# Kernel tuning notes

Hardware: AMD Instinct MI355X
Metric: run time of the kernel (lower is better)

## Reference

```python
import jax, jax.numpy as jnp
import numpy as np
import math

N_NODES = 100000
N_EDGES = 3200000
F_IN = 512
HID = 128
N_CLS = 16


def setup_inputs() -> dict:
    key = jax.random.key(0)
    k = jax.random.split(key, 6)
    x = jax.random.normal(k[0], (N_NODES, F_IN), dtype=jnp.float32)
    edge_index = jax.random.randint(k[1], (2, N_EDGES), 0, N_NODES, dtype=jnp.int32)
    W1 = jax.random.normal(k[2], (F_IN, HID), dtype=jnp.float32) / np.sqrt(F_IN)
    W2 = jax.random.normal(k[3], (HID, HID), dtype=jnp.float32) / np.sqrt(HID)
    W3 = jax.random.normal(k[4], (N_CLS, HID), dtype=jnp.float32) / np.sqrt(HID)
    b3 = jnp.zeros((N_CLS,), dtype=jnp.float32)
    return {"x": x, "edge_index": edge_index, "W1": W1, "W2": W2, "W3": W3, "b3": b3}


def _sym_norm(edge_index, num_nodes, dtype):
    # add self loops with fill_value = trunc(log2(average_node_degree))
    E = edge_index.shape[1]
    fill = float(math.trunc(math.log2(E / num_nodes)))
    loops = jnp.arange(num_nodes, dtype=edge_index.dtype)
    row = jnp.concatenate([edge_index[0], loops])
    col = jnp.concatenate([edge_index[1], loops])
    w = jnp.concatenate([jnp.ones((E,), dtype), jnp.full((num_nodes,), fill, dtype)])
    deg = jax.ops.segment_sum(w, row, num_segments=num_nodes)
    deg_inv_sqrt = jnp.where(deg > 0, jax.lax.rsqrt(deg), 0.0)
    norm = deg_inv_sqrt[row] * w * deg_inv_sqrt[col]
    return row, col, norm


def reference(x, edge_index, W1, W2, W3, b3):
    N = x.shape[0]
    row, col, norm = _sym_norm(edge_index, N, x.dtype)

    def gcn(h, W):
        h = h @ W                                   # [N, d_out]
        msg = norm[:, None] * h[col]                # gather + scale, [E', d_out]
        return jax.ops.segment_sum(msg, row, num_segments=N)

    h = jax.nn.relu(gcn(x, W1))      # layer 1 + srelu (threshold clamped at 0)
    h = gcn(h, W2)                   # layer 2
    # dropout p=0.5 is identity in eval mode
    return h @ W3.T + b3             # linear classifier [N, n_classes]
```

## Files before the change

### kernel.cpp

```cpp
#include <hip/hip_runtime.h>
#include <cmath>

typedef __attribute__((ext_vector_type(8))) short short8;
typedef __attribute__((ext_vector_type(8))) unsigned short ushort8;
typedef __attribute__((ext_vector_type(4))) float f32x4;
typedef __attribute__((ext_vector_type(2))) float f32x2;
typedef __attribute__((ext_vector_type(4))) unsigned int uint4v;
typedef __attribute__((ext_vector_type(2))) int int2v;

#define EPB 4096
#define BCAP 20480

__device__ inline float bf16_lo(unsigned int p) {
  union { unsigned int i; float f; } v; v.i = p << 16; return v.f;
}
__device__ inline float bf16_hi(unsigned int p) {
  union { unsigned int i; float f; } v; v.i = p & 0xffff0000u; return v.f;
}
__device__ inline f32x2 bf2(unsigned int p) {
  union { unsigned int i; float f; } lo, hi;
  lo.i = p << 16;
  hi.i = p & 0xffff0000u;
  return (f32x2){lo.f, hi.f};
}
__device__ inline float bf16u(unsigned short w) {
  union { unsigned int i; float f; } v; v.i = (unsigned int)w << 16; return v.f;
}
__device__ inline unsigned short f32_to_bf16(float f) {
  union { float f; unsigned int i; } v; v.f = f;
  unsigned int x = v.i;
  x += 0x7fffu + ((x >> 16) & 1u);
  return (unsigned short)(x >> 16);
}
__device__ inline f32x2 pk_add(f32x2 a, f32x2 b) {
  f32x2 d;
  asm("v_pk_add_f32 %0, %1, %2" : "=v"(d) : "v"(a), "v"(b));
  return d;
}

__global__ __launch_bounds__(256) void bin_k(const int* __restrict__ rows,
                                             const int* __restrict__ cols,
                                             int* __restrict__ bucket_cursor,
                                             unsigned int* __restrict__ binned, int E) {
  __shared__ int lhist[256];
  __shared__ int gbase[256];
  __shared__ int loff[256];
  const int t = threadIdx.x;
  const int base = blockIdx.x * EPB;
  lhist[t] = 0;
  __syncthreads();

  int bk[16];
  unsigned int pk[16];
#pragma unroll
  for (int j = 0; j < 16; ++j) {
    int e = base + j * 256 + t;
    if (e < E) {
      int r = rows[e];
      int c = cols[e];
      bk[j] = r >> 9;
      pk[j] = ((unsigned int)(r & 511) << 17) | (unsigned int)c;
      atomicAdd(&lhist[bk[j]], 1);
    } else {
      bk[j] = -1;
    }
  }
  __syncthreads();
  if (lhist[t] > 0) gbase[t] = atomicAdd(&bucket_cursor[t], lhist[t]);
  loff[t] = 0;
  __syncthreads();
#pragma unroll
  for (int j = 0; j < 16; ++j) {
    if (bk[j] >= 0) {
      int rank = gbase[bk[j]] + atomicAdd(&loff[bk[j]], 1);
      if (rank < BCAP) binned[(size_t)bk[j] * BCAP + rank] = pk[j];
    }
  }
}

__global__ __launch_bounds__(1024) void bucket_csr_k(const unsigned int* __restrict__ binned,
                                                     const int* __restrict__ bucket_cursor,
                                                     int2v* __restrict__ rowse,
                                                     float* __restrict__ dis,
                                                     int* __restrict__ col_sorted,
                                                     int* __restrict__ perm,
                                                     int N, float fill) {
  __shared__ int lcnt[512];
  __shared__ int lscan[512];
  __shared__ int dh[512];
  __shared__ int ds2[512];
  const int b = blockIdx.x;
  const int t = threadIdx.x;
  const int start = b * BCAP;
  int cnt = bucket_cursor[b];
  if (cnt > BCAP) cnt = BCAP;
  const int endb = start + cnt;
  const int rbase = b << 9;

  if (t < 512) lcnt[t] = 0;
  __syncthreads();
  for (int i = start + t; i < endb; i += 1024)
    atomicAdd(&lcnt[binned[i] >> 17], 1);
  __syncthreads();

  int v = (t < 512) ? lcnt[t] : 0;
  if (t < 512) lscan[t] = v;
  __syncthreads();
  for (int off = 1; off < 512; off <<= 1) {
    int add = (t < 512 && t >= off) ? lscan[t - off] : 0;
    __syncthreads();
    if (t < 512) lscan[t] += add;
    __syncthreads();
  }

  if (t < 512) {
    int excl = lscan[t] - v;
    int r = rbase + t;
    if (r < N) {
      rowse[r] = (int2v){start + excl, start + excl + v};
      float d = (float)v + fill;
      dis[r] = d > 0.f ? rsqrtf(d) : 0.f;
    }
    lcnt[t] = excl;
  }

  if (t < 512) dh[t] = 0;
  __syncthreads();
  int key = 0;
  if (t < 512) {
    key = 511 - (v < 511 ? v : 511);
    atomicAdd(&dh[key], 1);
  }
  __syncthreads();
  if (t < 512) ds2[t] = dh[t];
  __syncthreads();
  for (int off = 1; off < 512; off <<= 1) {
    int add = (t < 512 && t >= off) ? ds2[t - off] : 0;
    __syncthreads();
    if (t < 512) ds2[t] += add;
    __syncthreads();
  }
  int base2 = 0;
  if (t < 512) base2 = ds2[t] - dh[t];
  __syncthreads();
  if (t < 512) dh[t] = base2;
  __syncthreads();
  if (t < 512) {
    int rank = atomicAdd(&dh[key], 1);
    perm[(b << 9) + rank] = rbase + t;
  }
  __syncthreads();

  for (int i = start + t; i < endb; i += 1024) {
    unsigned int pk = binned[i];
    int rl = (int)(pk >> 17);
    int c = (int)(pk & 0x1FFFFu);
    int pos = atomicAdd(&lcnt[rl], 1);
    col_sorted[start + pos] = c;
  }
}

__global__ __launch_bounds__(256) void cast_w_k(const float* __restrict__ W1,
                                                const float* __restrict__ W2,
                                                const float* __restrict__ W3,
                                                unsigned short* __restrict__ W1t,
                                                unsigned short* __restrict__ W2t,
                                                unsigned short* __restrict__ W3b,
                                                int FIN) {
  int g = blockIdx.x * 256 + threadIdx.x;
  int n1 = FIN * 128;
  if (g < n1) {
    int n = g & 127, k = g >> 7;
    W1t[n * FIN + k] = f32_to_bf16(W1[(size_t)k * 128 + n]);
  } else if (g < n1 + 128 * 128) {
    int gg = g - n1;
    int n = gg & 127, k = gg >> 7;
    W2t[n * 128 + k] = f32_to_bf16(W2[k * 128 + n]);
  } else if (g < n1 + 128 * 128 + 16 * 128) {
    int gg = g - n1 - 128 * 128;
    W3b[gg] = f32_to_bf16(W3[gg]);
  }
}

__global__ __launch_bounds__(256) void gemm_k(const void* __restrict__ Aq, int a_is_f32,
                                              int M, int K,
                                              const unsigned short* __restrict__ Bt,
                                              const float* __restrict__ dis,
                                              unsigned short* __restrict__ C) {
  __shared__ unsigned short Al[128 * 40];
  __shared__ unsigned short Bl[128 * 40];
  const int t = threadIdx.x;
  const int bm = blockIdx.x * 128;
  const int lane = t & 63;
  const int wave = t >> 6;
  const int wm = (wave >> 1) * 64;
  const int wn = (wave & 1) * 64;
  const int l15 = lane & 15;
  const int l4 = lane >> 4;

  f32x4 acc[4][4];
#pragma unroll
  for (int a = 0; a < 4; ++a)
#pragma unroll
    for (int b = 0; b < 4; ++b) acc[a][b] = (f32x4){0.f, 0.f, 0.f, 0.f};

  const int am = t >> 1;
  const int ak = (t & 1) * 16;
  const int bn = t >> 1;
  const int bk = (t & 1) * 16;
  const int arow = bm + am;
  const bool arow_ok = arow < M;

  auto load_a = [&](int k0, ushort8& o0, ushort8& o1) {
    o0 = (ushort8){0, 0, 0, 0, 0, 0, 0, 0};
    o1 = (ushort8){0, 0, 0, 0, 0, 0, 0, 0};
    if (arow_ok) {
      if (a_is_f32) {
        const float* p = (const float*)Aq + (size_t)arow * K + k0 + ak;
#pragma unroll
        for (int j = 0; j < 8; ++j) o0[j] = f32_to_bf16(p[j]);
#pragma unroll
        for (int j = 0; j < 8; ++j) o1[j] = f32_to_bf16(p[8 + j]);
      } else {
        const unsigned short* p = (const unsigned short*)Aq + (size_t)arow * K + k0 + ak;
        o0 = *(const ushort8*)p;
        o1 = *(const ushort8*)(p + 8);
      }
    }
  };

  ushort8 av0, av1;
  load_a(0, av0, av1);
  ushort8 bv0 = *(const ushort8*)(Bt + (size_t)bn * K + bk);
  ushort8 bv1 = *(const ushort8*)(Bt + (size_t)bn * K + bk + 8);

  for (int k0 = 0; k0 < K; k0 += 32) {
    *(ushort8*)&Al[am * 40 + ak] = av0;
    *(ushort8*)&Al[am * 40 + ak + 8] = av1;
    *(ushort8*)&Bl[bn * 40 + bk] = bv0;
    *(ushort8*)&Bl[bn * 40 + bk + 8] = bv1;
    __syncthreads();

    const int kn = k0 + 32;
    if (kn < K) {
      load_a(kn, av0, av1);
      bv0 = *(const ushort8*)(Bt + (size_t)bn * K + kn + bk);
      bv1 = *(const ushort8*)(Bt + (size_t)bn * K + kn + bk + 8);
    }

    short8 af[4];
#pragma unroll
    for (int mt = 0; mt < 4; ++mt)
      af[mt] = *(const short8*)&Al[(wm + mt * 16 + l15) * 40 + l4 * 8];
#pragma unroll
    for (int nt = 0; nt < 4; ++nt) {
      short8 bfr = *(const short8*)&Bl[(wn + nt * 16 + l15) * 40 + l4 * 8];
#pragma unroll
      for (int mt = 0; mt < 4; ++mt)
        acc[mt][nt] = __builtin_amdgcn_mfma_f32_16x16x32_bf16(af[mt], bfr, acc[mt][nt], 0, 0, 0);
    }
    __syncthreads();
  }

#pragma unroll
  for (int mt = 0; mt < 4; ++mt) {
    int rbase = bm + wm + mt * 16 + l4 * 4;
#pragma unroll
    for (int r = 0; r < 4; ++r) {
      int row = rbase + r;
      if (row < M) {
        float dr = dis[row];
#pragma unroll
        for (int nt = 0; nt < 4; ++nt) {
          int col = wn + nt * 16 + l15;
          C[(size_t)row * 128 + col] = f32_to_bf16(acc[mt][nt][r] * dr);
        }
      }
    }
  }
}

__global__ __launch_bounds__(256) void agg_k(const unsigned short* __restrict__ hs,
                                             const int2v* __restrict__ rowse,
                                             const int* __restrict__ cols,
                                             const float* __restrict__ dis,
                                             const int* __restrict__ perm,
                                             unsigned short* __restrict__ out_bf,
                                             const unsigned short* __restrict__ W3b,
                                             const float* __restrict__ b3,
                                             float* __restrict__ fcout,
                                             int N, float fill, int mode) {
  const int q = blockIdx.x * 16 + (threadIdx.x >> 4);
  const unsigned int fl = threadIdx.x & 15;
  const int rid = perm[q];
  if (rid >= N) return;
  const char* __restrict__ hsc = (const char*)hs;
  const unsigned int flo = fl << 4;

  int2v se = rowse[rid];
  int e = se.x;
  const int end = se.y;

  f32x2 a0 = {0.f, 0.f}, a1 = {0.f, 0.f}, a2 = {0.f, 0.f}, a3 = {0.f, 0.f};

  for (; e + 8 <= end; e += 8) {
    unsigned int c0 = (unsigned int)cols[e];
    unsigned int c1 = (unsigned int)cols[e + 1];
    unsigned int c2 = (unsigned int)cols[e + 2];
    unsigned int c3 = (unsigned int)cols[e + 3];
    unsigned int c4 = (unsigned int)cols[e + 4];
    unsigned int c5 = (unsigned int)cols[e + 5];
    unsigned int c6 = (unsigned int)cols[e + 6];
    unsigned int c7 = (unsigned int)cols[e + 7];
    uint4v p0 = *(const uint4v*)(hsc + ((c0 << 8) | flo));
    uint4v p1 = *(const uint4v*)(hsc + ((c1 << 8) | flo));
    uint4v p2 = *(const uint4v*)(hsc + ((c2 << 8) | flo));
    uint4v p3 = *(const uint4v*)(hsc + ((c3 << 8) | flo));
    uint4v p4 = *(const uint4v*)(hsc + ((c4 << 8) | flo));
    uint4v p5 = *(const uint4v*)(hsc + ((c5 << 8) | flo));
    uint4v p6 = *(const uint4v*)(hsc + ((c6 << 8) | flo));
    uint4v p7 = *(const uint4v*)(hsc + ((c7 << 8) | flo));
    a0 = pk_add(a0, bf2(p0[0])); a1 = pk_add(a1, bf2(p0[1]));
    a2 = pk_add(a2, bf2(p0[2])); a3 = pk_add(a3, bf2(p0[3]));
    a0 = pk_add(a0, bf2(p1[0])); a1 = pk_add(a1, bf2(p1[1]));
    a2 = pk_add(a2, bf2(p1[2])); a3 = pk_add(a3, bf2(p1[3]));
    a0 = pk_add(a0, bf2(p2[0])); a1 = pk_add(a1, bf2(p2[1]));
    a2 = pk_add(a2, bf2(p2[2])); a3 = pk_add(a3, bf2(p2[3]));
    a0 = pk_add(a0, bf2(p3[0])); a1 = pk_add(a1, bf2(p3[1]));
    a2 = pk_add(a2, bf2(p3[2])); a3 = pk_add(a3, bf2(p3[3]));
    a0 = pk_add(a0, bf2(p4[0])); a1 = pk_add(a1, bf2(p4[1]));
    a2 = pk_add(a2, bf2(p4[2])); a3 = pk_add(a3, bf2(p4[3]));
    a0 = pk_add(a0, bf2(p5[0])); a1 = pk_add(a1, bf2(p5[1]));
    a2 = pk_add(a2, bf2(p5[2])); a3 = pk_add(a3, bf2(p5[3]));
    a0 = pk_add(a0, bf2(p6[0])); a1 = pk_add(a1, bf2(p6[1]));
    a2 = pk_add(a2, bf2(p6[2])); a3 = pk_add(a3, bf2(p6[3]));
    a0 = pk_add(a0, bf2(p7[0])); a1 = pk_add(a1, bf2(p7[1]));
    a2 = pk_add(a2, bf2(p7[2])); a3 = pk_add(a3, bf2(p7[3]));
  }
  for (; e + 4 <= end; e += 4) {
    unsigned int c0 = (unsigned int)cols[e];
    unsigned int c1 = (unsigned int)cols[e + 1];
    unsigned int c2 = (unsigned int)cols[e + 2];
    unsigned int c3 = (unsigned int)cols[e + 3];
    uint4v p0 = *(const uint4v*)(hsc + ((c0 << 8) | flo));
    uint4v p1 = *(const uint4v*)(hsc + ((c1 << 8) | flo));
    uint4v p2 = *(const uint4v*)(hsc + ((c2 << 8) | flo));
    uint4v p3 = *(const uint4v*)(hsc + ((c3 << 8) | flo));
    a0 = pk_add(a0, bf2(p0[0])); a1 = pk_add(a1, bf2(p0[1]));
    a2 = pk_add(a2, bf2(p0[2])); a3 = pk_add(a3, bf2(p0[3]));
    a0 = pk_add(a0, bf2(p1[0])); a1 = pk_add(a1, bf2(p1[1]));
    a2 = pk_add(a2, bf2(p1[2])); a3 = pk_add(a3, bf2(p1[3]));
    a0 = pk_add(a0, bf2(p2[0])); a1 = pk_add(a1, bf2(p2[1]));
    a2 = pk_add(a2, bf2(p2[2])); a3 = pk_add(a3, bf2(p2[3]));
    a0 = pk_add(a0, bf2(p3[0])); a1 = pk_add(a1, bf2(p3[1]));
    a2 = pk_add(a2, bf2(p3[2])); a3 = pk_add(a3, bf2(p3[3]));
  }
  for (; e < end; ++e) {
    unsigned int c = (unsigned int)cols[e];
    uint4v p = *(const uint4v*)(hsc + ((c << 8) | flo));
    a0 = pk_add(a0, bf2(p[0])); a1 = pk_add(a1, bf2(p[1]));
    a2 = pk_add(a2, bf2(p[2])); a3 = pk_add(a3, bf2(p[3]));
  }

  uint4v ps = *(const uint4v*)(hsc + (((unsigned int)rid << 8) | flo));
  float dr = dis[rid];
  float v[8];
  v[0] = dr * (a0.x + fill * bf16_lo(ps[0]));
  v[1] = dr * (a0.y + fill * bf16_hi(ps[0]));
  v[2] = dr * (a1.x + fill * bf16_lo(ps[1]));
  v[3] = dr * (a1.y + fill * bf16_hi(ps[1]));
  v[4] = dr * (a2.x + fill * bf16_lo(ps[2]));
  v[5] = dr * (a2.y + fill * bf16_hi(ps[2]));
  v[6] = dr * (a3.x + fill * bf16_lo(ps[3]));
  v[7] = dr * (a3.y + fill * bf16_hi(ps[3]));

  if (mode == 0) {
    uint4v o;
#pragma unroll
    for (int k = 0; k < 4; ++k) {
      float f0 = fmaxf(v[2 * k], 0.f);
      float f1 = fmaxf(v[2 * k + 1], 0.f);
      o[k] = ((unsigned int)f32_to_bf16(f1) << 16) | (unsigned int)f32_to_bf16(f0);
    }
    *(uint4v*)((char*)out_bf + (((unsigned int)rid << 8) | flo)) = o;
  } else {
    float p[16];
#pragma unroll
    for (int c = 0; c < 16; ++c) {
      ushort8 wr = *(const ushort8*)(W3b + c * 128 + fl * 8);
      float s = v[0] * bf16u(wr[0]);
      s = fmaf(v[1], bf16u(wr[1]), s);
      s = fmaf(v[2], bf16u(wr[2]), s);
      s = fmaf(v[3], bf16u(wr[3]), s);
      s = fmaf(v[4], bf16u(wr[4]), s);
      s = fmaf(v[5], bf16u(wr[5]), s);
      s = fmaf(v[6], bf16u(wr[6]), s);
      s = fmaf(v[7], bf16u(wr[7]), s);
      p[c] = s;
    }
#pragma unroll
    for (int m = 1; m <= 8; m <<= 1)
#pragma unroll
      for (int c = 0; c < 16; ++c) p[c] += __shfl_xor(p[c], m);
    fcout[(size_t)rid * 16 + fl] = p[fl] + b3[fl];
  }
}

extern "C" void kernel_launch(void* const* d_in, const int* in_sizes, int n_in,
                              void* d_out, int out_size, void* d_ws, size_t ws_size,
                              hipStream_t stream) {
  const float* x  = (const float*)d_in[0];
  const int* edge = (const int*)d_in[1];
  const float* W1 = (const float*)d_in[2];
  const float* W2 = (const float*)d_in[3];
  const float* W3 = (const float*)d_in[4];
  const float* b3 = (const float*)d_in[5];
  float* out = (float*)d_out;

  const int HID = 128;
  const int FIN = in_sizes[2] / HID;
  const int N   = in_sizes[0] / FIN;
  const int E   = in_sizes[1] / 2;
  const float fill = truncf(log2f((float)E / (float)N));

  char* w = (char*)d_ws;
  size_t off = 0;
  auto alloc = [&](size_t bytes) -> void* {
    void* p = w + off;
    off += (bytes + 255) & ~(size_t)255;
    return p;
  };
  const int NB = (N + 511) >> 9;
  float* dis      = (float*)alloc((size_t)N * 4);
  int2v* rowse    = (int2v*)alloc((size_t)N * 8);
  int* perm       = (int*)alloc((size_t)NB * 512 * 4);
  int* col_sorted = (int*)alloc((size_t)NB * BCAP * 4);
  int* bucket_cursor = (int*)alloc(256 * 4);
  unsigned int* binned = (unsigned int*)alloc((size_t)NB * BCAP * 4);
  unsigned short* W1t  = (unsigned short*)alloc((size_t)FIN * 128 * 2);
  unsigned short* W2t  = (unsigned short*)alloc(128 * 128 * 2);
  unsigned short* W3b  = (unsigned short*)alloc(16 * 128 * 2);
  unsigned short* bufA = (unsigned short*)alloc((size_t)N * 128 * 2);
  unsigned short* bufB = (unsigned short*)alloc((size_t)N * 128 * 2);

  const int* rows  = edge;
  const int* colsp = edge + E;

  hipMemsetAsync(bucket_cursor, 0, 256 * 4, stream);
  bin_k<<<(E + EPB - 1) / EPB, 256, 0, stream>>>(rows, colsp, bucket_cursor, binned, E);
  bucket_csr_k<<<NB, 1024, 0, stream>>>(binned, bucket_cursor, rowse, dis,
                                        col_sorted, perm, N, fill);
  const int castN = FIN * 128 + 128 * 128 + 16 * 128;
  cast_w_k<<<(castN + 255) / 256, 256, 0, stream>>>(W1, W2, W3, W1t, W2t, W3b, FIN);

  const int gm = (N + 127) / 128;
  gemm_k<<<gm, 256, 0, stream>>>(x, 1, N, FIN, W1t, dis, bufA);
  agg_k<<<NB * 32, 256, 0, stream>>>(bufA, rowse, col_sorted, dis, perm, bufB,
                                     W3b, b3, out, N, fill, 0);
  gemm_k<<<gm, 256, 0, stream>>>(bufB, 0, N, HID, W2t, dis, bufA);
  agg_k<<<NB * 32, 256, 0, stream>>>(bufA, rowse, col_sorted, dis, perm, bufB,
                                     W3b, b3, out, N, fill, 1);
}
```

Measured before the change: 651.3 us.

## Use wave-shuffle scans, packed bf16 converts, vector loads and nontemporal hints

Replaces the shared-memory Hillis-Steele scans in the CSR build kernel with a wave-shuffle scan followed by a small cross-wave pass, cutting barrier count. The GEMM's fp32 A-tile load becomes vectorized 16-byte loads with hardware packed bf16 conversion instead of scalar loads and software rounding. The aggregation kernel uses nontemporal loads for perm, row ranges and column indices, a packed bf16 convert and a nontemporal store for the output. These target instruction count and cache pollution, but the nontemporal store of layer-1 output may evict data that layer 2 reads again.

After: 670.7 us. 1.03x slower.

```diff
diff --git a/kernel.cpp b/kernel.cpp
--- a/kernel.cpp
+++ b/kernel.cpp
@@ -31,6 +31,11 @@
   unsigned int x = v.i;
   x += 0x7fffu + ((x >> 16) & 1u);
   return (unsigned short)(x >> 16);
+}
+__device__ inline unsigned int cvt_pk_bf16(float a, float b) {
+  unsigned int r;
+  asm("v_cvt_pk_bf16_f32 %0, %1, %2" : "=v"(r) : "v"(a), "v"(b));
+  return r;
 }
 __device__ inline f32x2 pk_add(f32x2 a, f32x2 b) {
   f32x2 d;
@@ -86,9 +91,8 @@
                                                      int* __restrict__ perm,
                                                      int N, float fill) {
   __shared__ int lcnt[512];
-  __shared__ int lscan[512];
   __shared__ int dh[512];
-  __shared__ int ds2[512];
+  __shared__ int wsum[16];
   const int b = blockIdx.x;
   const int t = threadIdx.x;
   const int start = b * BCAP;
@@ -97,6 +101,29 @@
   const int endb = start + cnt;
   const int rbase = b << 9;
 
+  auto scan512 = [&](int v) -> int {
+    int x = v;
+#pragma unroll
+    for (int d = 1; d < 64; d <<= 1) {
+      int u = __shfl_up(x, d, 64);
+      if ((t & 63) >= d) x += u;
+    }
+    if (t < 512 && (t & 63) == 63) wsum[t >> 6] = x;
+    __syncthreads();
+    if (t < 64) {
+      int s = (t < 8) ? wsum[t] : 0;
+#pragma unroll
+      for (int d = 1; d < 8; d <<= 1) {
+        int u = __shfl_up(s, d, 64);
+        if (t >= d) s += u;
+      }
+      if (t < 8) wsum[t] = s;
+    }
+    __syncthreads();
+    int off = (t >= 64 && t < 512) ? wsum[(t >> 6) - 1] : 0;
+    return x + off;
+  };
+
   if (t < 512) lcnt[t] = 0;
   __syncthreads();
   for (int i = start + t; i < endb; i += 1024)
@@ -104,17 +131,9 @@
   __syncthreads();
 
   int v = (t < 512) ? lcnt[t] : 0;
-  if (t < 512) lscan[t] = v;
-  __syncthreads();
-  for (int off = 1; off < 512; off <<= 1) {
-    int add = (t < 512 && t >= off) ? lscan[t - off] : 0;
-    __syncthreads();
-    if (t < 512) lscan[t] += add;
-    __syncthreads();
-  }
-
+  int incl = scan512(v);
   if (t < 512) {
-    int excl = lscan[t] - v;
+    int excl = incl - v;
     int r = rbase + t;
     if (r < N) {
       rowse[r] = (int2v){start + excl, start + excl + v};
@@ -123,6 +142,7 @@
     }
     lcnt[t] = excl;
   }
+  __syncthreads();
 
   if (t < 512) dh[t] = 0;
   __syncthreads();
@@ -132,18 +152,9 @@
     atomicAdd(&dh[key], 1);
   }
   __syncthreads();
-  if (t < 512) ds2[t] = dh[t];
-  __syncthreads();
-  for (int off = 1; off < 512; off <<= 1) {
-    int add = (t < 512 && t >= off) ? ds2[t - off] : 0;
-    __syncthreads();
-    if (t < 512) ds2[t] += add;
-    __syncthreads();
-  }
-  int base2 = 0;
-  if (t < 512) base2 = ds2[t] - dh[t];
-  __syncthreads();
-  if (t < 512) dh[t] = base2;
+  int hv = (t < 512) ? dh[t] : 0;
+  int hincl = scan512(hv);
+  if (t < 512) dh[t] = hincl - hv;
   __syncthreads();
   if (t < 512) {
     int rank = atomicAdd(&dh[key], 1);
@@ -217,10 +228,21 @@
     if (arow_ok) {
       if (a_is_f32) {
         const float* p = (const float*)Aq + (size_t)arow * K + k0 + ak;
-#pragma unroll
-        for (int j = 0; j < 8; ++j) o0[j] = f32_to_bf16(p[j]);
-#pragma unroll
-        for (int j = 0; j < 8; ++j) o1[j] = f32_to_bf16(p[8 + j]);
+        f32x4 f0 = *(const f32x4*)(p);
+        f32x4 f1 = *(const f32x4*)(p + 4);
+        f32x4 f2 = *(const f32x4*)(p + 8);
+        f32x4 f3 = *(const f32x4*)(p + 12);
+        union { unsigned int u[4]; ushort8 v8; } c0, c1;
+        c0.u[0] = cvt_pk_bf16(f0[0], f0[1]);
+        c0.u[1] = cvt_pk_bf16(f0[2], f0[3]);
+        c0.u[2] = cvt_pk_bf16(f1[0], f1[1]);
+        c0.u[3] = cvt_pk_bf16(f1[2], f1[3]);
+        c1.u[0] = cvt_pk_bf16(f2[0], f2[1]);
+        c1.u[1] = cvt_pk_bf16(f2[2], f2[3]);
+        c1.u[2] = cvt_pk_bf16(f3[0], f3[1]);
+        c1.u[3] = cvt_pk_bf16(f3[2], f3[3]);
+        o0 = c0.v8;
+        o1 = c1.v8;
       } else {
         const unsigned short* p = (const unsigned short*)Aq + (size_t)arow * K + k0 + ak;
         o0 = *(const ushort8*)p;
@@ -292,26 +314,26 @@
                                              int N, float fill, int mode) {
   const int q = blockIdx.x * 16 + (threadIdx.x >> 4);
   const unsigned int fl = threadIdx.x & 15;
-  const int rid = perm[q];
+  const int rid = __builtin_nontemporal_load(&perm[q]);
   if (rid >= N) return;
   const char* __restrict__ hsc = (const char*)hs;
   const unsigned int flo = fl << 4;
 
-  int2v se = rowse[rid];
+  int2v se = __builtin_nontemporal_load(&rowse[rid]);
   int e = se.x;
   const int end = se.y;
 
   f32x2 a0 = {0.f, 0.f}, a1 = {0.f, 0.f}, a2 = {0.f, 0.f}, a3 = {0.f, 0.f};
 
   for (; e + 8 <= end; e += 8) {
-    unsigned int c0 = (unsigned int)cols[e];
-    unsigned int c1 = (unsigned int)cols[e + 1];
-    unsigned int c2 = (unsigned int)cols[e + 2];
-    unsigned int c3 = (unsigned int)cols[e + 3];
-    unsigned int c4 = (unsigned int)cols[e + 4];
-    unsigned int c5 = (unsigned int)cols[e + 5];
-    unsigned int c6 = (unsigned int)cols[e + 6];
-    unsigned int c7 = (unsigned int)cols[e + 7];
+    unsigned int c0 = (unsigned int)__builtin_nontemporal_load(&cols[e]);
+    unsigned int c1 = (unsigned int)__builtin_nontemporal_load(&cols[e + 1]);
+    unsigned int c2 = (unsigned int)__builtin_nontemporal_load(&cols[e + 2]);
+    unsigned int c3 = (unsigned int)__builtin_nontemporal_load(&cols[e + 3]);
+    unsigned int c4 = (unsigned int)__builtin_nontemporal_load(&cols[e + 4]);
+    unsigned int c5 = (unsigned int)__builtin_nontemporal_load(&cols[e + 5]);
+    unsigned int c6 = (unsigned int)__builtin_nontemporal_load(&cols[e + 6]);
+    unsigned int c7 = (unsigned int)__builtin_nontemporal_load(&cols[e + 7]);
     uint4v p0 = *(const uint4v*)(hsc + ((c0 << 8) | flo));
     uint4v p1 = *(const uint4v*)(hsc + ((c1 << 8) | flo));
     uint4v p2 = *(const uint4v*)(hsc + ((c2 << 8) | flo));
@@ -338,10 +360,10 @@
     a2 = pk_add(a2, bf2(p7[2])); a3 = pk_add(a3, bf2(p7[3]));
   }
   for (; e + 4 <= end; e += 4) {
-    unsigned int c0 = (unsigned int)cols[e];
-    unsigned int c1 = (unsigned int)cols[e + 1];
-    unsigned int c2 = (unsigned int)cols[e + 2];
-    unsigned int c3 = (unsigned int)cols[e + 3];
+    unsigned int c0 = (unsigned int)__builtin_nontemporal_load(&cols[e]);
+    unsigned int c1 = (unsigned int)__builtin_nontemporal_load(&cols[e + 1]);
+    unsigned int c2 = (unsigned int)__builtin_nontemporal_load(&cols[e + 2]);
+    unsigned int c3 = (unsigned int)__builtin_nontemporal_load(&cols[e + 3]);
     uint4v p0 = *(const uint4v*)(hsc + ((c0 << 8) | flo));
     uint4v p1 = *(const uint4v*)(hsc + ((c1 << 8) | flo));
     uint4v p2 = *(const uint4v*)(hsc + ((c2 << 8) | flo));
@@ -356,7 +378,7 @@
     a2 = pk_add(a2, bf2(p3[2])); a3 = pk_add(a3, bf2(p3[3]));
   }
   for (; e < end; ++e) {
-    unsigned int c = (unsigned int)cols[e];
+    unsigned int c = (unsigned int)__builtin_nontemporal_load(&cols[e]);
     uint4v p = *(const uint4v*)(hsc + ((c << 8) | flo));
     a0 = pk_add(a0, bf2(p[0])); a1 = pk_add(a1, bf2(p[1]));
     a2 = pk_add(a2, bf2(p[2])); a3 = pk_add(a3, bf2(p[3]));
@@ -380,9 +402,9 @@
     for (int k = 0; k < 4; ++k) {
       float f0 = fmaxf(v[2 * k], 0.f);
       float f1 = fmaxf(v[2 * k + 1], 0.f);
-      o[k] = ((unsigned int)f32_to_bf16(f1) << 16) | (unsigned int)f32_to_bf16(f0);
-    }
-    *(uint4v*)((char*)out_bf + (((unsigned int)rid << 8) | flo)) = o;
+      o[k] = cvt_pk_bf16(f0, f1);
+    }
+    __builtin_nontemporal_store(o, (uint4v*)((char*)out_bf + (((unsigned int)rid << 8) | flo)));
   } else {
     float p[16];
 #pragma unroll
```
